# Kernel tuning notes

Measured on AMD Instinct MI355X. Metric: run time of the kernel, lower is better.

Reference implementation:

```python
import jax, jax.numpy as jnp
import numpy as np

S, R, CM, CZ, C, H = 128, 256, 256, 128, 32, 8
EPS = 1e-5


def layer_norm(x, w, b):
    mu = jnp.mean(x, axis=-1, keepdims=True)
    var = jnp.mean(jnp.square(x - mu), axis=-1, keepdims=True)
    return (x - mu) * jax.lax.rsqrt(var + EPS) * w + b


def setup_inputs() -> dict:
    key = jax.random.key(0)
    ks = jax.random.split(key, 10)
    s = 0.02
    return {
        "m": jax.random.normal(ks[0], (S, R, CM), jnp.float32),
        "z": jax.random.normal(ks[1], (R, R, CZ), jnp.float32),
        "ln_m_w": jnp.ones((CM,), jnp.float32),
        "ln_m_b": jnp.zeros((CM,), jnp.float32),
        "ln_z_w": jnp.ones((CZ,), jnp.float32),
        "ln_z_b": jnp.zeros((CZ,), jnp.float32),
        "Wz": jax.random.normal(ks[2], (CZ, H), jnp.float32) * s,
        "Wq": jax.random.normal(ks[3], (CM, H * C), jnp.float32) * s,
        "Wk": jax.random.normal(ks[4], (CM, H * C), jnp.float32) * s,
        "Wv": jax.random.normal(ks[5], (CM, H * C), jnp.float32) * s,
        "Wg": jax.random.normal(ks[6], (CM, H * C), jnp.float32) * s,
        "bg": jnp.ones((H * C,), jnp.float32),
        "Wo": jax.random.normal(ks[7], (H * C, CM), jnp.float32) * s,
        "bo": jnp.zeros((CM,), jnp.float32),
    }


def reference(m, z, ln_m_w, ln_m_b, ln_z_w, ln_z_b, Wz, Wq, Wk, Wv, Wg, bg, Wo, bo):
    mn = layer_norm(m, ln_m_w, ln_m_b)              # [S,R,CM]
    zn = layer_norm(z, ln_z_w, ln_z_b)              # [R,R,CZ]
    bias = jnp.einsum('qkz,zh->hqk', zn, Wz)        # [H,R,R] pair bias
    q = (mn @ Wq).reshape(S, R, H, C) * (C ** -0.5)
    k = (mn @ Wk).reshape(S, R, H, C)
    v = (mn @ Wv).reshape(S, R, H, C)
    logits = jnp.einsum('sqhc,skhc->shqk', q, k) + bias[None]  # [S,H,R,R]
    a = jax.nn.softmax(logits, axis=-1)
    o = jnp.einsum('shqk,skhc->sqhc', a, v)         # [S,R,H,C]
    g = jax.nn.sigmoid(mn @ Wg + bg).reshape(S, R, H, C)
    return (g * o).reshape(S, R, H * C) @ Wo + bo   # [S,R,CM]
```

## Files before the change

kernel.cpp:

```cpp
#include <hip/hip_runtime.h>
#include <math.h>

#define S_DIM 128
#define R_DIM 256
#define CM_DIM 256
#define CZ_DIM 128
#define C_DIM 32
#define H_DIM 8
#define HC_DIM 256
#define LN_EPS 1e-5f
#define ZPAD 132
#define HSZ 1048576
#define BIAS_SCALE 16384.0f
#define BIAS_INV (1.0f / 16384.0f)

typedef _Float16 half8 __attribute__((ext_vector_type(8)));
typedef _Float16 half4 __attribute__((ext_vector_type(4)));
typedef float f32x4 __attribute__((ext_vector_type(4)));
typedef short short4v __attribute__((ext_vector_type(4)));
typedef short short8v __attribute__((ext_vector_type(8)));

__device__ __forceinline__ float wave_sum(float v) {
#pragma unroll
    for (int off = 32; off > 0; off >>= 1) v += __shfl_down(v, off);
    return v;
}

__device__ __forceinline__ void gload16(const _Float16* src, _Float16* dst) {
    __builtin_amdgcn_global_load_lds((const __attribute__((address_space(1))) void*)src,
                                     (__attribute__((address_space(3))) void*)dst, 16, 0, 0);
}

__global__ __launch_bounds__(256) void convert_w_kernel(const float* __restrict__ Wq,
                                                        const float* __restrict__ Wk,
                                                        const float* __restrict__ Wv,
                                                        const float* __restrict__ Wg,
                                                        const float* __restrict__ Wo,
                                                        _Float16* __restrict__ w3) {
    int kb = blockIdx.x;
    int mat = blockIdx.y;
    const float* src = (mat == 0) ? Wq : (mat == 1) ? Wk : (mat == 2) ? Wv : (mat == 3) ? Wg : Wo;
    int n = threadIdx.x;
    _Float16 tmp[32];
#pragma unroll
    for (int kk = 0; kk < 32; kk++)
        tmp[kk] = (_Float16)src[(size_t)(kb * 32 + kk) * 256 + n];
    half8* dst = (half8*)(w3 + (size_t)mat * 65536 + (size_t)kb * 8192 + (size_t)n * 32);
#pragma unroll
    for (int i = 0; i < 4; i++) dst[i] = *(half8*)&tmp[i * 8];
}

__global__ __launch_bounds__(64) void prep_wz_kernel(const float* __restrict__ w,
                                                     const float* __restrict__ b,
                                                     const float* __restrict__ Wz,
                                                     float* __restrict__ u_g,
                                                     float* __restrict__ UB) {
    int lane = threadIdx.x;
    float w0 = w[lane], w1 = w[lane + 64];
    float b0 = b[lane], b1 = b[lane + 64];
#pragma unroll
    for (int h = 0; h < H_DIM; h++) {
        float wz0 = Wz[lane * H_DIM + h], wz1 = Wz[(lane + 64) * H_DIM + h];
        float u0 = w0 * wz0, u1 = w1 * wz1;
        u_g[h * ZPAD + lane] = u0;
        u_g[h * ZPAD + lane + 64] = u1;
        float U = wave_sum(u0 + u1);
        float B = wave_sum(b0 * wz0 + b1 * wz1);
        if (lane == 0) { UB[h] = U; UB[8 + h] = B; }
    }
}

__global__ __launch_bounds__(64) void ln_m_kernel(const float* __restrict__ m,
                                                  const float* __restrict__ w,
                                                  const float* __restrict__ b,
                                                  _Float16* __restrict__ mn) {
    int row = blockIdx.x;
    int t = threadIdx.x;
    const float4* mrow = (const float4*)(m + (size_t)row * CM_DIM);
    float4 x = mrow[t];
    float s = x.x + x.y + x.z + x.w;
    float ss = x.x * x.x + x.y * x.y + x.z * x.z + x.w * x.w;
    s = wave_sum(s);
    ss = wave_sum(ss);
    s = __shfl(s, 0);
    ss = __shfl(ss, 0);
    float mean = s * (1.0f / CM_DIM);
    float var = ss * (1.0f / CM_DIM) - mean * mean;
    float rsig = rsqrtf(var + LN_EPS);
    float4 wv = ((const float4*)w)[t];
    float4 bv = ((const float4*)b)[t];
    half4 o;
    o[0] = (_Float16)((x.x - mean) * rsig * wv.x + bv.x);
    o[1] = (_Float16)((x.y - mean) * rsig * wv.y + bv.y);
    o[2] = (_Float16)((x.z - mean) * rsig * wv.z + bv.z);
    o[3] = (_Float16)((x.w - mean) * rsig * wv.w + bv.w);
    *(half4*)(mn + (size_t)row * CM_DIM + t * 4) = o;
}

__global__ __launch_bounds__(256) void ln_z_bias_kernel(const float* __restrict__ z,
                                                        const float* __restrict__ u_g,
                                                        const float* __restrict__ UB,
                                                        short* __restrict__ bias_i) {
    __shared__ __align__(16) float zt[64 * ZPAD];
    __shared__ __align__(16) float ut[8 * ZPAD];
    __shared__ float UBs[16];
    int tid = threadIdx.x;
    int row0 = blockIdx.x * 64;
    for (int i = tid; i < 8 * ZPAD; i += 256) ut[i] = u_g[i];
    if (tid < 16) UBs[tid] = UB[tid];
    const float4* zsrc = (const float4*)(z + (size_t)row0 * CZ_DIM);
#pragma unroll
    for (int i = 0; i < 8; i++) {
        int idx = tid + i * 256;
        float4 v = zsrc[idx];
        int r = idx >> 5, c4 = (idx & 31) * 4;
        *(float4*)&zt[r * ZPAD + c4] = v;
    }
    __syncthreads();
    int r = tid >> 2, p = tid & 3;
    const float* zr = &zt[r * ZPAD];
    const float* u0p = &ut[p * ZPAD];
    const float* u1p = &ut[(p + 4) * ZPAD];
    float s = 0.f, ss = 0.f, a0 = 0.f, a1 = 0.f;
#pragma unroll
    for (int c = 0; c < CZ_DIM; c += 4) {
        float4 x = *(const float4*)&zr[c];
        float4 uu0 = *(const float4*)&u0p[c];
        float4 uu1 = *(const float4*)&u1p[c];
        s += x.x + x.y + x.z + x.w;
        ss += x.x * x.x + x.y * x.y + x.z * x.z + x.w * x.w;
        a0 += x.x * uu0.x + x.y * uu0.y + x.z * uu0.z + x.w * uu0.w;
        a1 += x.x * uu1.x + x.y * uu1.y + x.z * uu1.z + x.w * uu1.w;
    }
    float mu = s * (1.0f / CZ_DIM);
    float var = ss * (1.0f / CZ_DIM) - mu * mu;
    float rsig = rsqrtf(var + LN_EPS);
    int row = row0 + r;
    float b0v = rsig * (a0 - mu * UBs[p]) + UBs[8 + p];
    float b1v = rsig * (a1 - mu * UBs[4 + p]) + UBs[12 + p];
    int i0 = (int)rintf(b0v * BIAS_SCALE);
    int i1 = (int)rintf(b1v * BIAS_SCALE);
    i0 = i0 > 32767 ? 32767 : (i0 < -32768 ? -32768 : i0);
    i1 = i1 > 32767 ? 32767 : (i1 < -32768 ? -32768 : i1);
    bias_i[(size_t)p * 65536 + row] = (short)i0;
    bias_i[(size_t)(p + 4) * 65536 + row] = (short)i1;
}

__global__ __launch_bounds__(256, 3) void proj_mfma_kernel(const _Float16* __restrict__ A,
                                                           const _Float16* __restrict__ w3,
                                                           const float* __restrict__ bg,
                                                           _Float16* __restrict__ qh,
                                                           _Float16* __restrict__ kh,
                                                           _Float16* __restrict__ vh,
                                                           _Float16* __restrict__ gh) {
    __shared__ _Float16 As[64 * 256];
    __shared__ _Float16 Os[64 * 128];
    int m0 = blockIdx.x * 64;
    int col0 = blockIdx.y * 128;
    int tid = threadIdx.x, lane = tid & 63, wave = tid >> 6;
    int lrow = lane & 15, g = lane >> 4, lk8 = g * 8;
    int wr = wave >> 1, wc = wave & 1;

#pragma unroll
    for (int i = 0; i < 8; i++) {
        int row = i * 8 + (tid >> 5);
        int c = (tid & 31) ^ (row & 7);
        gload16(A + (size_t)(m0 + row) * 256 + c * 8, As + (size_t)(i * 256 + tid) * 8);
    }
    __syncthreads();

    const float qscale = 0.17677669529663687f;
    for (int mat = 0; mat < 4; mat++) {
        const _Float16* W = w3 + (size_t)mat * 65536;
        f32x4 acc[2][4];
#pragma unroll
        for (int i = 0; i < 2; i++)
#pragma unroll
            for (int j = 0; j < 4; j++) acc[i][j] = (f32x4){0.f, 0.f, 0.f, 0.f};
#pragma unroll
        for (int kb = 0; kb < 8; kb++) {
            half8 af[2], bf[4];
#pragma unroll
            for (int mf = 0; mf < 2; mf++) {
                int row = wr * 32 + mf * 16 + lrow;
                af[mf] = *(half8*)&As[row * 256 + (((kb * 4 + g) ^ (row & 7)) * 8)];
            }
#pragma unroll
            for (int nf = 0; nf < 4; nf++)
                bf[nf] = *(const half8*)(W + (size_t)kb * 8192 +
                                         (size_t)(col0 + wc * 64 + nf * 16 + lrow) * 32 + lk8);
#pragma unroll
            for (int mf = 0; mf < 2; mf++)
#pragma unroll
                for (int nf = 0; nf < 4; nf++)
                    acc[mf][nf] = __builtin_amdgcn_mfma_f32_16x16x32_f16(af[mf], bf[nf], acc[mf][nf], 0, 0, 0);
        }
        __syncthreads();
#pragma unroll
        for (int mf = 0; mf < 2; mf++)
#pragma unroll
            for (int nf = 0; nf < 4; nf++)
#pragma unroll
                for (int ri = 0; ri < 4; ri++) {
                    int srow = wr * 32 + mf * 16 + g * 4 + ri;
                    int scol = wc * 64 + nf * 16 + lrow;
                    float v = acc[mf][nf][ri];
                    if (mat == 0) v *= qscale;
                    if (mat == 3) v = 1.0f / (1.0f + __expf(-(v + bg[col0 + scol])));
                    Os[srow * 128 + scol] = (_Float16)v;
                }
        __syncthreads();
        if (mat < 3) {
            _Float16* Out = (mat == 0) ? qh : (mat == 1) ? kh : vh;
#pragma unroll
            for (int j = 0; j < 4; j++) {
                int hh = (col0 >> 5) + j;
                int row = tid >> 2, cOff = (tid & 3) * 8;
                half8 v8 = *(half8*)&Os[row * 128 + j * 32 + cOff];
                *(half8*)(Out + (size_t)hh * HSZ + (size_t)(m0 + row) * 32 + cOff) = v8;
            }
        } else {
#pragma unroll
            for (int i = 0; i < 4; i++) {
                int c2 = tid + i * 256;
                int row = c2 >> 4, cOff = (c2 & 15) * 8;
                half8 v8 = *(half8*)&Os[row * 128 + cOff];
                *(half8*)(gh + (size_t)(m0 + row) * 256 + col0 + cOff) = v8;
            }
        }
    }
}

__global__ __launch_bounds__(512, 1) void attn_mfma_kernel(const _Float16* __restrict__ qh,
                                                           const _Float16* __restrict__ kh,
                                                           const _Float16* __restrict__ vh,
                                                           const _Float16* __restrict__ gh,
                                                           const short* __restrict__ bias_i,
                                                           _Float16* __restrict__ oh) {
    __shared__ short bias_s[256][264];
    __shared__ _Float16 K_s[64][40];
    __shared__ _Float16 VT_s[32][72];
    int h = blockIdx.x, sg = blockIdx.y;
    int tid = threadIdx.x;
    int lane = tid & 63, wave = tid >> 6;
    int lrow = lane & 15, g = lane >> 4, lk8 = g * 8;
    int qw = wave * 32;

    const short* bsrc = bias_i + (size_t)h * 65536;
#pragma unroll
    for (int i = 0; i < 16; i++) {
        int e = (tid + i * 512) * 8;
        short8v v = *(const short8v*)(bsrc + e);
        *(short8v*)&bias_s[e >> 8][e & 255] = v;
    }

    const _Float16* qbase = qh + (size_t)h * HSZ;
    const _Float16* kbase = kh + (size_t)h * HSZ;
    const _Float16* vbase = vh + (size_t)h * HSZ;
    _Float16* obase = oh + (size_t)h * HSZ;

    bool isK = (wave < 4);
    int key = (tid & 255) >> 2, koff = (tid & 3) * 8;
    int vkey = tid & 63, vc0 = ((tid >> 6) & 3) * 8;

    for (int si = 0; si < 4; si++) {
        int s = sg * 4 + si;
        half8 qfr[2];
#pragma unroll
        for (int qf = 0; qf < 2; qf++)
            qfr[qf] = *(const half8*)(qbase + (size_t)(s * 256 + qw + qf * 16 + lrow) * 32 + lk8);

        f32x4 oaccT[2][2];
        float m_run[2], l_run[2];
#pragma unroll
        for (int qf = 0; qf < 2; qf++) {
            oaccT[qf][0] = (f32x4){0.f, 0.f, 0.f, 0.f};
            oaccT[qf][1] = (f32x4){0.f, 0.f, 0.f, 0.f};
            m_run[qf] = -1e30f;
            l_run[qf] = 0.f;
        }

        half8 stg;
        if (isK) stg = *(const half8*)(kbase + (size_t)(s * 256 + key) * 32 + koff);
        else     stg = *(const half8*)(vbase + (size_t)(s * 256 + vkey) * 32 + vc0);

        for (int kb = 0; kb < 4; kb++) {
            __syncthreads();
            if (isK) {
                *(half8*)&K_s[key][koff] = stg;
            } else {
#pragma unroll
                for (int j = 0; j < 8; j++) VT_s[vc0 + j][vkey] = stg[j];
            }
            if (kb < 3) {
                int nk = (kb + 1) * 64;
                if (isK) stg = *(const half8*)(kbase + (size_t)(s * 256 + nk + key) * 32 + koff);
                else     stg = *(const half8*)(vbase + (size_t)(s * 256 + nk + vkey) * 32 + vc0);
            }
            __syncthreads();

            half8 kfr[4];
#pragma unroll
            for (int kf = 0; kf < 4; kf++) kfr[kf] = *(half8*)&K_s[kf * 16 + lrow][lk8];

#pragma unroll
            for (int qf = 0; qf < 2; qf++) {
                f32x4 sf[4];
#pragma unroll
                for (int kf = 0; kf < 4; kf++) {
                    f32x4 zero = (f32x4){0.f, 0.f, 0.f, 0.f};
                    sf[kf] = __builtin_amdgcn_mfma_f32_16x16x32_f16(kfr[kf], qfr[qf], zero, 0, 0, 0);
                }
                int q = qw + qf * 16 + lrow;
#pragma unroll
                for (int kf = 0; kf < 4; kf++) {
                    short4v bh = *(short4v*)&bias_s[q][kb * 64 + kf * 16 + 4 * g];
#pragma unroll
                    for (int ri = 0; ri < 4; ri++) sf[kf][ri] += (float)bh[ri] * BIAS_INV;
                }
                float tm = -1e30f;
#pragma unroll
                for (int kf = 0; kf < 4; kf++)
#pragma unroll
                    for (int ri = 0; ri < 4; ri++) tm = fmaxf(tm, sf[kf][ri]);
                tm = fmaxf(tm, __shfl_xor(tm, 16));
                tm = fmaxf(tm, __shfl_xor(tm, 32));
                float nm = fmaxf(m_run[qf], tm);
                float sc = __expf(m_run[qf] - nm);
                m_run[qf] = nm;
                oaccT[qf][0] *= sc;
                oaccT[qf][1] *= sc;
                float p[4][4];
                float rs = 0.f;
#pragma unroll
                for (int kf = 0; kf < 4; kf++)
#pragma unroll
                    for (int ri = 0; ri < 4; ri++) {
                        float pv = __expf(sf[kf][ri] - nm);
                        p[kf][ri] = pv;
                        rs += pv;
                    }
                rs += __shfl_xor(rs, 16);
                rs += __shfl_xor(rs, 32);
                l_run[qf] = l_run[qf] * sc + rs;
                unsigned w8[8];
#pragma unroll
                for (int kf = 0; kf < 4; kf++)
#pragma unroll
                    for (int t = 0; t < 2; t++) {
                        union { _Float16 hh[2]; unsigned u; } pk;
                        pk.hh[0] = (_Float16)p[kf][2 * t];
                        pk.hh[1] = (_Float16)p[kf][2 * t + 1];
                        w8[2 * kf + t] = pk.u;
                    }
#pragma unroll
                for (int ks = 0; ks < 2; ks++) {
                    union { unsigned u[4]; half8 h8; } pb;
#pragma unroll
                    for (int u = 0; u < 4; u++) {
                        int srcl = ((g & 1) * 2 + (u >> 1)) * 16 + lrow;
                        unsigned lo_sh = (unsigned)__shfl((int)w8[4 * ks + (u & 1)], srcl);
                        unsigned hi_sh = (unsigned)__shfl((int)w8[4 * ks + (u & 1) + 2], srcl);
                        pb.u[u] = (g >> 1) ? hi_sh : lo_sh;
                    }
#pragma unroll
                    for (int cf = 0; cf < 2; cf++) {
                        half8 va = *(half8*)&VT_s[cf * 16 + lrow][ks * 32 + lk8];
                        oaccT[qf][cf] =
                            __builtin_amdgcn_mfma_f32_16x16x32_f16(va, pb.h8, oaccT[qf][cf], 0, 0, 0);
                    }
                }
            }
        }
#pragma unroll
        for (int qf = 0; qf < 2; qf++) {
            float inv = 1.0f / l_run[qf];
            int q = qw + qf * 16 + lrow;
#pragma unroll
            for (int cf = 0; cf < 2; cf++) {
                half4 gv4 = *(const half4*)(gh + (size_t)(s * 256 + q) * 256 + h * 32 + cf * 16 + 4 * g);
                half4 o4;
#pragma unroll
                for (int ri = 0; ri < 4; ri++)
                    o4[ri] = (_Float16)(oaccT[qf][cf][ri] * inv * (float)gv4[ri]);
                *(half4*)(obase + (size_t)(s * 256 + q) * 32 + cf * 16 + 4 * g) = o4;
            }
        }
    }
}

__global__ __launch_bounds__(256, 4) void out_mfma_kernel(const _Float16* __restrict__ oh,
                                                          const _Float16* __restrict__ w3o,
                                                          const float* __restrict__ bo,
                                                          float* __restrict__ out) {
    __shared__ _Float16 As[64 * 256];
    int m0 = blockIdx.x * 64;
    int col0 = blockIdx.y * 128;
    int tid = threadIdx.x, lane = tid & 63, wave = tid >> 6;
    int lrow = lane & 15, g = lane >> 4, lk8 = g * 8;
    int wr = wave >> 1, wc = wave & 1;

#pragma unroll
    for (int i = 0; i < 8; i++) {
        int row = i * 8 + (tid >> 5);
        int cc = (tid & 31) ^ (row & 7);
        gload16(oh + (size_t)(cc >> 2) * HSZ + (size_t)(m0 + row) * 32 + (cc & 3) * 8,
                As + (size_t)(i * 256 + tid) * 8);
    }
    __syncthreads();

    f32x4 acc[2][4];
#pragma unroll
    for (int i = 0; i < 2; i++)
#pragma unroll
        for (int j = 0; j < 4; j++) acc[i][j] = (f32x4){0.f, 0.f, 0.f, 0.f};
#pragma unroll
    for (int kb = 0; kb < 8; kb++) {
        half8 af[2], bf[4];
#pragma unroll
        for (int mf = 0; mf < 2; mf++) {
            int row = wr * 32 + mf * 16 + lrow;
            af[mf] = *(half8*)&As[row * 256 + (((kb * 4 + g) ^ (row & 7)) * 8)];
        }
#pragma unroll
        for (int nf = 0; nf < 4; nf++)
            bf[nf] = *(const half8*)(w3o + (size_t)kb * 8192 +
                                     (size_t)(col0 + wc * 64 + nf * 16 + lrow) * 32 + lk8);
#pragma unroll
        for (int mf = 0; mf < 2; mf++)
#pragma unroll
            for (int nf = 0; nf < 4; nf++)
                acc[mf][nf] = __builtin_amdgcn_mfma_f32_16x16x32_f16(af[mf], bf[nf], acc[mf][nf], 0, 0, 0);
    }
#pragma unroll
    for (int mf = 0; mf < 2; mf++)
#pragma unroll
        for (int nf = 0; nf < 4; nf++)
#pragma unroll
            for (int ri = 0; ri < 4; ri++) {
                int row = m0 + wr * 32 + mf * 16 + g * 4 + ri;
                int col = col0 + wc * 64 + nf * 16 + lrow;
                out[(size_t)row * 256 + col] = acc[mf][nf][ri] + bo[col];
            }
}

extern "C" void kernel_launch(void* const* d_in, const int* in_sizes, int n_in,
                              void* d_out, int out_size, void* d_ws, size_t ws_size,
                              hipStream_t stream) {
    const float* m = (const float*)d_in[0];
    const float* z = (const float*)d_in[1];
    const float* ln_m_w = (const float*)d_in[2];
    const float* ln_m_b = (const float*)d_in[3];
    const float* ln_z_w = (const float*)d_in[4];
    const float* ln_z_b = (const float*)d_in[5];
    const float* Wz = (const float*)d_in[6];
    const float* Wq = (const float*)d_in[7];
    const float* Wk = (const float*)d_in[8];
    const float* Wv = (const float*)d_in[9];
    const float* Wg = (const float*)d_in[10];
    const float* bg = (const float*)d_in[11];
    const float* Wo = (const float*)d_in[12];
    const float* bo = (const float*)d_in[13];
    float* out = (float*)d_out;

    const size_t NE = (size_t)S_DIM * R_DIM * CM_DIM;
    _Float16* hb = (_Float16*)d_ws;
    _Float16* mn_h = hb;
    _Float16* qh = hb + NE;
    _Float16* kh = hb + 2 * NE;
    _Float16* vh = hb + 3 * NE;
    _Float16* gh = hb + 4 * NE;
    _Float16* oh = hb + 5 * NE;
    _Float16* w3 = hb + 6 * NE;
    float* u_g = (float*)(hb + 6 * NE + 5 * 65536);
    float* UB = u_g + 8 * ZPAD;
    short* bias_i = (short*)(UB + 16);

    hipLaunchKernelGGL(convert_w_kernel, dim3(8, 5), dim3(256), 0, stream,
                       Wq, Wk, Wv, Wg, Wo, w3);
    hipLaunchKernelGGL(prep_wz_kernel, dim3(1), dim3(64), 0, stream,
                       ln_z_w, ln_z_b, Wz, u_g, UB);
    hipLaunchKernelGGL(ln_m_kernel, dim3(S_DIM * R_DIM), dim3(64), 0, stream,
                       m, ln_m_w, ln_m_b, mn_h);
    hipLaunchKernelGGL(ln_z_bias_kernel, dim3(1024), dim3(256), 0, stream,
                       z, u_g, UB, bias_i);
    hipLaunchKernelGGL(proj_mfma_kernel, dim3(512, 2), dim3(256), 0, stream,
                       mn_h, w3, bg, qh, kh, vh, gh);
    hipLaunchKernelGGL(attn_mfma_kernel, dim3(H_DIM, 32), dim3(512), 0, stream,
                       qh, kh, vh, gh, bias_i, oh);
    hipLaunchKernelGGL(out_mfma_kernel, dim3(512, 2), dim3(256), 0, stream,
                       oh, w3 + 4 * 65536, bo, out);
}
```

Baseline: 139.5 us.

## Stage weight tiles in LDS and loop persistently over row tiles in GEMMs

```diff
diff --git a/kernel.cpp b/kernel.cpp
--- a/kernel.cpp
+++ b/kernel.cpp
@@ -146,32 +146,46 @@
     bias_i[(size_t)(p + 4) * 65536 + row] = (short)i1;
 }
 
-__global__ __launch_bounds__(256, 3) void proj_mfma_kernel(const _Float16* __restrict__ A,
+__global__ __launch_bounds__(256, 1) void proj_mfma_kernel(const _Float16* __restrict__ A,
                                                            const _Float16* __restrict__ w3,
                                                            const float* __restrict__ bg,
                                                            _Float16* __restrict__ qh,
                                                            _Float16* __restrict__ kh,
                                                            _Float16* __restrict__ vh,
                                                            _Float16* __restrict__ gh) {
+    __shared__ _Float16 Bs[8 * 128 * 32];
     __shared__ _Float16 As[64 * 256];
-    __shared__ _Float16 Os[64 * 128];
-    int m0 = blockIdx.x * 64;
-    int col0 = blockIdx.y * 128;
+    __shared__ _Float16 Os[64 * 132];
+    int mg = blockIdx.x;
+    int yb = blockIdx.y;
+    int mat = yb >> 1, col0 = (yb & 1) * 128;
     int tid = threadIdx.x, lane = tid & 63, wave = tid >> 6;
     int lrow = lane & 15, g = lane >> 4, lk8 = g * 8;
     int wr = wave >> 1, wc = wave & 1;
-
+    const _Float16* Wb = w3 + (size_t)mat * 65536;
+    _Float16* Out = (mat == 0) ? qh : (mat == 1) ? kh : (mat == 2) ? vh : gh;
+    const float qscale = 0.17677669529663687f;
+
+#pragma unroll
+    for (int i = 0; i < 16; i++) {
+        int j = tid + i * 256;
+        int kb = j >> 9, jj = j & 511;
+        int n = jj >> 2, c = jj & 3;
+        int csrc = c ^ ((n >> 1) & 3);
+        gload16(Wb + (size_t)kb * 8192 + (size_t)(col0 + n) * 32 + csrc * 8,
+                Bs + (size_t)j * 8);
+    }
+    int r0 = mg * 1024;
 #pragma unroll
     for (int i = 0; i < 8; i++) {
         int row = i * 8 + (tid >> 5);
         int c = (tid & 31) ^ (row & 7);
-        gload16(A + (size_t)(m0 + row) * 256 + c * 8, As + (size_t)(i * 256 + tid) * 8);
+        gload16(A + (size_t)(r0 + row) * 256 + c * 8, As + (size_t)(i * 256 + tid) * 8);
     }
     __syncthreads();
 
-    const float qscale = 0.17677669529663687f;
-    for (int mat = 0; mat < 4; mat++) {
-        const _Float16* W = w3 + (size_t)mat * 65536;
+    for (int t = 0; t < 16; t++) {
+        int rt = mg * 1024 + t * 64;
         f32x4 acc[2][4];
 #pragma unroll
         for (int i = 0; i < 2; i++)
@@ -186,9 +200,10 @@
                 af[mf] = *(half8*)&As[row * 256 + (((kb * 4 + g) ^ (row & 7)) * 8)];
             }
 #pragma unroll
-            for (int nf = 0; nf < 4; nf++)
-                bf[nf] = *(const half8*)(W + (size_t)kb * 8192 +
-                                         (size_t)(col0 + wc * 64 + nf * 16 + lrow) * 32 + lk8);
+            for (int nf = 0; nf < 4; nf++) {
+                int n = wc * 64 + nf * 16 + lrow;
+                bf[nf] = *(half8*)&Bs[(size_t)(kb * 512 + n * 4 + (g ^ ((n >> 1) & 3))) * 8];
+            }
 #pragma unroll
             for (int mf = 0; mf < 2; mf++)
 #pragma unroll
@@ -196,6 +211,15 @@
                     acc[mf][nf] = __builtin_amdgcn_mfma_f32_16x16x32_f16(af[mf], bf[nf], acc[mf][nf], 0, 0, 0);
         }
         __syncthreads();
+        if (t < 15) {
+            int rn = mg * 1024 + (t + 1) * 64;
+#pragma unroll
+            for (int i = 0; i < 8; i++) {
+                int row = i * 8 + (tid >> 5);
+                int c = (tid & 31) ^ (row & 7);
+                gload16(A + (size_t)(rn + row) * 256 + c * 8, As + (size_t)(i * 256 + tid) * 8);
+            }
+        }
 #pragma unroll
         for (int mf = 0; mf < 2; mf++)
 #pragma unroll
@@ -207,27 +231,27 @@
                     float v = acc[mf][nf][ri];
                     if (mat == 0) v *= qscale;
                     if (mat == 3) v = 1.0f / (1.0f + __expf(-(v + bg[col0 + scol])));
-                    Os[srow * 128 + scol] = (_Float16)v;
+                    Os[srow * 132 + scol] = (_Float16)v;
                 }
         __syncthreads();
         if (mat < 3) {
-            _Float16* Out = (mat == 0) ? qh : (mat == 1) ? kh : vh;
 #pragma unroll
             for (int j = 0; j < 4; j++) {
                 int hh = (col0 >> 5) + j;
                 int row = tid >> 2, cOff = (tid & 3) * 8;
-                half8 v8 = *(half8*)&Os[row * 128 + j * 32 + cOff];
-                *(half8*)(Out + (size_t)hh * HSZ + (size_t)(m0 + row) * 32 + cOff) = v8;
+                half8 v8 = *(half8*)&Os[row * 132 + j * 32 + cOff];
+                *(half8*)(Out + (size_t)hh * HSZ + (size_t)(rt + row) * 32 + cOff) = v8;
             }
         } else {
 #pragma unroll
             for (int i = 0; i < 4; i++) {
                 int c2 = tid + i * 256;
                 int row = c2 >> 4, cOff = (c2 & 15) * 8;
-                half8 v8 = *(half8*)&Os[row * 128 + cOff];
-                *(half8*)(gh + (size_t)(m0 + row) * 256 + col0 + cOff) = v8;
-            }
-        }
+                half8 v8 = *(half8*)&Os[row * 132 + cOff];
+                *(half8*)(gh + (size_t)(rt + row) * 256 + col0 + cOff) = v8;
+            }
+        }
+        __syncthreads();
     }
 }
 
@@ -389,59 +413,86 @@
     }
 }
 
-__global__ __launch_bounds__(256, 4) void out_mfma_kernel(const _Float16* __restrict__ oh,
+__global__ __launch_bounds__(256, 1) void out_mfma_kernel(const _Float16* __restrict__ oh,
                                                           const _Float16* __restrict__ w3o,
                                                           const float* __restrict__ bo,
                                                           float* __restrict__ out) {
+    __shared__ _Float16 Bs[8 * 128 * 32];
     __shared__ _Float16 As[64 * 256];
-    int m0 = blockIdx.x * 64;
+    int mg = blockIdx.x;
     int col0 = blockIdx.y * 128;
     int tid = threadIdx.x, lane = tid & 63, wave = tid >> 6;
-    int lrow = lane & 15, g = lane >> 4, lk8 = g * 8;
+    int lrow = lane & 15, g = lane >> 4;
     int wr = wave >> 1, wc = wave & 1;
 
+#pragma unroll
+    for (int i = 0; i < 16; i++) {
+        int j = tid + i * 256;
+        int kb = j >> 9, jj = j & 511;
+        int n = jj >> 2, c = jj & 3;
+        int csrc = c ^ ((n >> 1) & 3);
+        gload16(w3o + (size_t)kb * 8192 + (size_t)(col0 + n) * 32 + csrc * 8,
+                Bs + (size_t)j * 8);
+    }
+    int r0 = mg * 256;
 #pragma unroll
     for (int i = 0; i < 8; i++) {
         int row = i * 8 + (tid >> 5);
         int cc = (tid & 31) ^ (row & 7);
-        gload16(oh + (size_t)(cc >> 2) * HSZ + (size_t)(m0 + row) * 32 + (cc & 3) * 8,
+        gload16(oh + (size_t)(cc >> 2) * HSZ + (size_t)(r0 + row) * 32 + (cc & 3) * 8,
                 As + (size_t)(i * 256 + tid) * 8);
     }
     __syncthreads();
 
-    f32x4 acc[2][4];
-#pragma unroll
-    for (int i = 0; i < 2; i++)
-#pragma unroll
-        for (int j = 0; j < 4; j++) acc[i][j] = (f32x4){0.f, 0.f, 0.f, 0.f};
-#pragma unroll
-    for (int kb = 0; kb < 8; kb++) {
-        half8 af[2], bf[4];
-#pragma unroll
-        for (int mf = 0; mf < 2; mf++) {
-            int row = wr * 32 + mf * 16 + lrow;
-            af[mf] = *(half8*)&As[row * 256 + (((kb * 4 + g) ^ (row & 7)) * 8)];
-        }
-#pragma unroll
-        for (int nf = 0; nf < 4; nf++)
-            bf[nf] = *(const half8*)(w3o + (size_t)kb * 8192 +
-                                     (size_t)(col0 + wc * 64 + nf * 16 + lrow) * 32 + lk8);
+    for (int t = 0; t < 4; t++) {
+        int rt = mg * 256 + t * 64;
+        f32x4 acc[2][4];
+#pragma unroll
+        for (int i = 0; i < 2; i++)
+#pragma unroll
+            for (int j = 0; j < 4; j++) acc[i][j] = (f32x4){0.f, 0.f, 0.f, 0.f};
+#pragma unroll
+        for (int kb = 0; kb < 8; kb++) {
+            half8 af[2], bf[4];
+#pragma unroll
+            for (int mf = 0; mf < 2; mf++) {
+                int row = wr * 32 + mf * 16 + lrow;
+                af[mf] = *(half8*)&As[row * 256 + (((kb * 4 + g) ^ (row & 7)) * 8)];
+            }
+#pragma unroll
+            for (int nf = 0; nf < 4; nf++) {
+                int n = wc * 64 + nf * 16 + lrow;
+                bf[nf] = *(half8*)&Bs[(size_t)(kb * 512 + n * 4 + (g ^ ((n >> 1) & 3))) * 8];
+            }
+#pragma unroll
+            for (int mf = 0; mf < 2; mf++)
+#pragma unroll
+                for (int nf = 0; nf < 4; nf++)
+                    acc[mf][nf] = __builtin_amdgcn_mfma_f32_16x16x32_f16(af[mf], bf[nf], acc[mf][nf], 0, 0, 0);
+        }
+        __syncthreads();
+        if (t < 3) {
+            int rn = mg * 256 + (t + 1) * 64;
+#pragma unroll
+            for (int i = 0; i < 8; i++) {
+                int row = i * 8 + (tid >> 5);
+                int cc = (tid & 31) ^ (row & 7);
+                gload16(oh + (size_t)(cc >> 2) * HSZ + (size_t)(rn + row) * 32 + (cc & 3) * 8,
+                        As + (size_t)(i * 256 + tid) * 8);
+            }
+        }
 #pragma unroll
         for (int mf = 0; mf < 2; mf++)
 #pragma unroll
             for (int nf = 0; nf < 4; nf++)
-                acc[mf][nf] = __builtin_amdgcn_mfma_f32_16x16x32_f16(af[mf], bf[nf], acc[mf][nf], 0, 0, 0);
-    }
-#pragma unroll
-    for (int mf = 0; mf < 2; mf++)
-#pragma unroll
-        for (int nf = 0; nf < 4; nf++)
-#pragma unroll
-            for (int ri = 0; ri < 4; ri++) {
-                int row = m0 + wr * 32 + mf * 16 + g * 4 + ri;
-                int col = col0 + wc * 64 + nf * 16 + lrow;
-                out[(size_t)row * 256 + col] = acc[mf][nf][ri] + bo[col];
-            }
+#pragma unroll
+                for (int ri = 0; ri < 4; ri++) {
+                    int row = rt + wr * 32 + mf * 16 + g * 4 + ri;
+                    int col = col0 + wc * 64 + nf * 16 + lrow;
+                    out[(size_t)row * 256 + col] = acc[mf][nf][ri] + bo[col];
+                }
+        __syncthreads();
+    }
 }
 
 extern "C" void kernel_launch(void* const* d_in, const int* in_sizes, int n_in,
@@ -484,10 +535,10 @@
                        m, ln_m_w, ln_m_b, mn_h);
     hipLaunchKernelGGL(ln_z_bias_kernel, dim3(1024), dim3(256), 0, stream,
                        z, u_g, UB, bias_i);
-    hipLaunchKernelGGL(proj_mfma_kernel, dim3(512, 2), dim3(256), 0, stream,
+    hipLaunchKernelGGL(proj_mfma_kernel, dim3(32, 8), dim3(256), 0, stream,
                        mn_h, w3, bg, qh, kh, vh, gh);
     hipLaunchKernelGGL(attn_mfma_kernel, dim3(H_DIM, 32), dim3(512), 0, stream,
                        qh, kh, vh, gh, bias_i, oh);
-    hipLaunchKernelGGL(out_mfma_kernel, dim3(512, 2), dim3(256), 0, stream,
+    hipLaunchKernelGGL(out_mfma_kernel, dim3(128, 2), dim3(256), 0, stream,
                        oh, w3 + 4 * 65536, bo, out);
 }
```

Measured after the change: 180.7 us. 1.3x slower.
